# Kernel optimization log

Hardware: AMD Instinct MI355X
Metric: run time of the kernel (lower is better)

Reference implementation:

```python
import jax, jax.numpy as jnp
import numpy as np

T, N = 500, 20000
DT = 0.1
REST_CA = 0.0

PNAMES = ['decay_ca', 'rho_ca', 'p__tau', 'p__scale', 'p__mdp', 'q__tau', 'q__scale',
          'q__mdp', 'n__tau', 'n__scale', 'n__mdp', 'f__tau', 'f__scale', 'f__mdp',
          'e__tau', 'e__scale', 'e__mdp', 'h__alpha', 'h__scale', 'h__mdp',
          'C_m', 'g_Ca', 'g_Ks', 'g_Kf', 'g_L', 'E_Ca', 'E_K', 'E_L']
DEFAULT = {'decay_ca': 110.0, 'rho_ca': 0.23, 'p__tau': 100.0, 'p__scale': 7.43,
           'p__mdp': -8.05, 'q__tau': 150.0, 'q__scale': -9.97, 'q__mdp': -15.6,
           'n__tau': 25.0, 'n__scale': 15.9, 'n__mdp': 19.9, 'f__tau': 151.0,
           'f__scale': -5.03, 'f__mdp': 25.2, 'e__tau': 10.0, 'e__scale': 6.75,
           'e__mdp': -3.36, 'h__alpha': 0.282, 'h__scale': -1.0, 'h__mdp': 6.42,
           'C_m': 20.0, 'g_Ca': 3.0, 'g_Ks': 10.0, 'g_Kf': 0.07, 'g_L': 0.005,
           'E_Ca': 20.0, 'E_K': -60.0, 'E_L': -60.0}
# initial state: V, p, q, n, e, f, cac
INIT_STATE = [-50.0, 0.0, 0.95, 0.0, 0.0, 1.0, 1e-07]


def setup_inputs() -> dict:
    key = jax.random.key(0)
    # injected current per timestep and neuron (uA/cm^2)
    i_inj = jax.random.normal(key, (T, N), dtype=jnp.float32) * 2.0 + 5.0
    x0 = jnp.broadcast_to(jnp.asarray(INIT_STATE, dtype=jnp.float32)[:, None], (7, N))
    params = jnp.asarray([DEFAULT[k] for k in PNAMES], dtype=jnp.float32)
    return {'i_inj': i_inj, 'x0': x0, 'params': params}


def _simulate(i_inj, x0, params):
    P = {k: params[i] for i, k in enumerate(PNAMES)}
    dt = jnp.float32(DT)

    def inf(V, r):
        return jax.nn.sigmoid((V - P[r + '__mdp']) / P[r + '__scale'])

    def gate(x, V, r):
        tau = P[r + '__tau']
        return tau * dt / (tau + dt) * (x / dt + inf(V, r) / tau)

    def step(X, i):
        V, p, q, n, e, f, cac = X  # each [N]
        h = 1.0 + (jax.nn.sigmoid((cac - P['h__mdp']) / P['h__scale']) - 1.0) * P['h__alpha']
        i_ca = P['g_Ca'] * e ** 2 * f * h * (V - P['E_Ca'])
        i_ks = P['g_Ks'] * n * (V - P['E_K'])
        i_kf = P['g_Kf'] * p ** 4 * q * (V - P['E_K'])
        i_l = P['g_L'] * (V - P['E_L'])
        V = V + (i - i_ca - i_ks - i_kf - i_l) / P['C_m'] * dt
        # cac update uses I_Ca recomputed with the *updated* V (as in source)
        i_ca2 = P['g_Ca'] * e ** 2 * f * h * (V - P['E_Ca'])
        cac = cac + (-i_ca2 * P['rho_ca'] - (cac - REST_CA) / P['decay_ca']) * dt
        p = gate(p, V, 'p')
        q = gate(q, V, 'q')
        e = gate(e, V, 'e')
        f = gate(f, V, 'f')
        n = gate(n, V, 'n')
        Xn = jnp.stack([V, p, q, n, e, f, cac], 0)
        return Xn, Xn

    _, traj = jax.lax.scan(step, x0, i_inj)
    return traj  # [T, 7, N]


def reference(i_inj, x0, params):
    return _simulate(i_inj, x0, params)
```

## Files before the change

### kernel.cpp

```cpp
#include <hip/hip_runtime.h>
#include <hip/hip_bf16.h>


#define TSTEPS 500
#define NNEUR  20000
#define DTS    0.1f
#define LOG2E  1.442695040888963f

__device__ __forceinline__ float hw_exp2(float x) { return __builtin_amdgcn_exp2f(x); }
__device__ __forceinline__ float hw_rcp(float x)  { return __builtin_amdgcn_rcpf(x); }

__global__ __launch_bounds__(64, 1)
void hh_kernel(const float* __restrict__ i_inj,
               const float* __restrict__ x0,
               const float* __restrict__ prm,
               float* __restrict__ out)
{
    const int n = blockIdx.x * 64 + threadIdx.x;
    if (n >= NNEUR) return;

    const float decay_ca = prm[0],  rho_ca  = prm[1];
    const float p_tau = prm[2],  p_scale = prm[3],  p_mdp = prm[4];
    const float q_tau = prm[5],  q_scale = prm[6],  q_mdp = prm[7];
    const float n_tau = prm[8],  n_scale = prm[9],  n_mdp = prm[10];
    const float f_tau = prm[11], f_scale = prm[12], f_mdp = prm[13];
    const float e_tau = prm[14], e_scale = prm[15], e_mdp = prm[16];
    const float h_alpha = prm[17], h_scale = prm[18], h_mdp = prm[19];
    const float C_m = prm[20], g_Ca = prm[21], g_Ks = prm[22];
    const float g_Kf = prm[23], g_L = prm[24];
    const float E_Ca = prm[25], E_K = prm[26], E_L = prm[27];

    const float kV    = DTS / C_m;
    const float cLEL  = g_L * E_L;
    const float cKeep = 1.0f - DTS / decay_ca;
    const float cRho  = rho_ca * DTS;

    const float isH = 1.0f / h_scale;
    const float zaH = -LOG2E * isH, zbH = h_mdp * isH * LOG2E;
    const float aG  = h_alpha * g_Ca;
    const float bG  = (1.0f - h_alpha) * g_Ca;

#define GATECONST(r, tau, scale, mdp)                                          \
    const float cf_##r = (tau) * DTS / ((tau) + DTS);                          \
    const float A_##r  = cf_##r / DTS;                                         \
    const float B_##r  = cf_##r / (tau);                                       \
    const float za##r  = -LOG2E / (scale);                                     \
    const float zb##r  = (mdp) * LOG2E / (scale);
    GATECONST(p, p_tau, p_scale, p_mdp)
    GATECONST(q, q_tau, q_scale, q_mdp)
    GATECONST(n, n_tau, n_scale, n_mdp)
    GATECONST(f, f_tau, f_scale, f_mdp)
    GATECONST(e, e_tau, e_scale, e_mdp)
#undef GATECONST

    float V   = x0[0 * NNEUR + n];
    float p   = x0[1 * NNEUR + n];
    float q   = x0[2 * NNEUR + n];
    float nn  = x0[3 * NNEUR + n];
    float e   = x0[4 * NNEUR + n];
    float f   = x0[5 * NNEUR + n];
    float cac = x0[6 * NNEUR + n];

    float* const oV = out + 0 * NNEUR;
    float* const oP = out + 1 * NNEUR;
    float* const oQ = out + 2 * NNEUR;
    float* const oN = out + 3 * NNEUR;
    float* const oE = out + 4 * NNEUR;
    float* const oF = out + 5 * NNEUR;
    float* const oC = out + 6 * NNEUR;
    unsigned boff = (unsigned)n * 4u;
    const unsigned BSTEP = 7u * NNEUR * 4u;
    unsigned ioff = (unsigned)n * 4u;
    const unsigned ISTEP = (unsigned)NNEUR * 4u;

#define LD(off)  (*(const float*)((const char*)i_inj + (off)))
#define ST(ptr)  (*(float*)((char*)(ptr) + boff))

#define HH_STEP(cur)                                                           \
    {                                                                          \
                                      \
        const float hs  = hw_rcp(1.0f + hw_exp2(fmaf(cac, zaH, zbH)));         \
        const float hg  = fmaf(hs, aG, bG);                        \
        const float geh = (e * e) * (f * hg);                                  \
        const float p2  = p * p;                                               \
        const float g   = fmaf(g_Kf, (p2 * p2) * q, g_Ks * nn);                \
        const float gtot = geh + g + g_L;                                      \
        const float t3  = fmaf(g, E_K, fmaf(geh, E_Ca, (cur) + cLEL));         \
        const float num = fmaf(-gtot, V, t3);                                  \
        V = fmaf(num, kV, V);                                                  \
                                               \
        const float ica2 = geh * (V - E_Ca);                                   \
        cac = fmaf(cac, cKeep, -(ica2 * cRho));                                \
                                                       \
        const float sp = hw_rcp(1.0f + hw_exp2(fmaf(V, zap, zbp)));            \
        const float sq = hw_rcp(1.0f + hw_exp2(fmaf(V, zaq, zbq)));            \
        const float se = hw_rcp(1.0f + hw_exp2(fmaf(V, zae, zbe)));            \
        const float sf = hw_rcp(1.0f + hw_exp2(fmaf(V, zaf, zbf)));            \
        const float sn = hw_rcp(1.0f + hw_exp2(fmaf(V, zan, zbn)));            \
        p  = fmaf(A_p, p,  B_p * sp);                                          \
        q  = fmaf(A_q, q,  B_q * sq);                                          \
        e  = fmaf(A_e, e,  B_e * se);                                          \
        f  = fmaf(A_f, f,  B_f * sf);                                          \
        nn = fmaf(A_n, nn, B_n * sn);                                          \
        ST(oV) = V;  ST(oP) = p;  ST(oQ) = q;  ST(oN) = nn;                    \
        ST(oE) = e;  ST(oF) = f;  ST(oC) = cac;                                \
        boff += BSTEP;                                                         \
    }

    float buf[8];
#pragma unroll
    for (int j = 0; j < 8; ++j)
        buf[j] = LD(ioff + (unsigned)j * ISTEP);
    ioff += 8u * ISTEP;

    for (int t0 = 0; t0 < TSTEPS - 8; t0 += 8) {
        float nbuf[8];
#pragma unroll
        for (int j = 0; j < 8; ++j) {
            unsigned o = ioff + (unsigned)j * ISTEP;
            const unsigned omax = (unsigned)(TSTEPS - 1) * ISTEP + (unsigned)n * 4u;
            o = o < omax ? o : omax;
            nbuf[j] = LD(o);
        }
        ioff += 8u * ISTEP;
#pragma unroll
        for (int j = 0; j < 8; ++j)
            HH_STEP(buf[j]);
#pragma unroll
        for (int j = 0; j < 8; ++j)
            buf[j] = nbuf[j];
    }

#pragma unroll
    for (int j = 0; j < 4; ++j)
        HH_STEP(buf[j]);

#undef HH_STEP
#undef LD
#undef ST
}

extern "C" void kernel_launch(void* const* d_in, const int* in_sizes, int n_in,
                              void* d_out, int out_size, void* d_ws, size_t ws_size,
                              hipStream_t stream) {
    const float* i_inj  = (const float*)d_in[0];
    const float* x0     = (const float*)d_in[1];
    const float* params = (const float*)d_in[2];
    float* out = (float*)d_out;

    const int block = 64;
    const int grid  = (NNEUR + block - 1) / block;
    hipLaunchKernelGGL(hh_kernel, dim3(grid), dim3(block), 0, stream,
                       i_inj, x0, params, out);
}
```

Before: 360.8 us.

## Process four neurons per thread to interleave independent recurrence chains

Each thread now integrates four neurons spaced NT apart, interleaving their time steps so independent dependency chains overlap in the pipeline. The grid shrinks fourfold, and the input prefetch depth drops from 8 to 4 steps with a uniform loop. This trades occupancy and CU coverage (far fewer waves than CUs) for instruction-level parallelism inside each wave.

```diff
diff --git a/kernel.cpp b/kernel.cpp
--- a/kernel.cpp
+++ b/kernel.cpp
@@ -4,6 +4,8 @@
 
 #define TSTEPS 500
 #define NNEUR  20000
+#define KN     4
+#define NT     (NNEUR / KN)
 #define DTS    0.1f
 #define LOG2E  1.442695040888963f
 
@@ -17,7 +19,7 @@
                float* __restrict__ out)
 {
     const int n = blockIdx.x * 64 + threadIdx.x;
-    if (n >= NNEUR) return;
+    if (n >= NT) return;
 
     const float decay_ca = prm[0],  rho_ca  = prm[1];
     const float p_tau = prm[2],  p_scale = prm[3],  p_mdp = prm[4];
@@ -53,13 +55,18 @@
     GATECONST(e, e_tau, e_scale, e_mdp)
 #undef GATECONST
 
-    float V   = x0[0 * NNEUR + n];
-    float p   = x0[1 * NNEUR + n];
-    float q   = x0[2 * NNEUR + n];
-    float nn  = x0[3 * NNEUR + n];
-    float e   = x0[4 * NNEUR + n];
-    float f   = x0[5 * NNEUR + n];
-    float cac = x0[6 * NNEUR + n];
+    float V[KN], P[KN], Q[KN], NN[KN], E[KN], F[KN], C[KN];
+#pragma unroll
+    for (int k = 0; k < KN; ++k) {
+        const int nk = n + k * NT;
+        V[k]  = x0[0 * NNEUR + nk];
+        P[k]  = x0[1 * NNEUR + nk];
+        Q[k]  = x0[2 * NNEUR + nk];
+        NN[k] = x0[3 * NNEUR + nk];
+        E[k]  = x0[4 * NNEUR + nk];
+        F[k]  = x0[5 * NNEUR + nk];
+        C[k]  = x0[6 * NNEUR + nk];
+    }
 
     float* const oV = out + 0 * NNEUR;
     float* const oP = out + 1 * NNEUR;
@@ -68,72 +75,80 @@
     float* const oE = out + 4 * NNEUR;
     float* const oF = out + 5 * NNEUR;
     float* const oC = out + 6 * NNEUR;
-    unsigned boff = (unsigned)n * 4u;
+
+    const unsigned ISTEP = (unsigned)NNEUR * 4u;
     const unsigned BSTEP = 7u * NNEUR * 4u;
-    unsigned ioff = (unsigned)n * 4u;
-    const unsigned ISTEP = (unsigned)NNEUR * 4u;
+    unsigned bo[KN];
+    unsigned i0[KN];
+#pragma unroll
+    for (int k = 0; k < KN; ++k) {
+        bo[k] = (unsigned)(n + k * NT) * 4u;
+        i0[k] = (unsigned)(n + k * NT) * 4u;
+    }
 
-#define LD(off)  (*(const float*)((const char*)i_inj + (off)))
-#define ST(ptr)  (*(float*)((char*)(ptr) + boff))
+#define LD(off)      (*(const float*)((const char*)i_inj + (off)))
+#define ST(ptr, off) (*(float*)((char*)(ptr) + (off)))
 
-#define HH_STEP(cur)                                                           \
+#define HH_STEP(k, cur)                                                        \
     {                                                                          \
-                                      \
-        const float hs  = hw_rcp(1.0f + hw_exp2(fmaf(cac, zaH, zbH)));         \
-        const float hg  = fmaf(hs, aG, bG);                        \
-        const float geh = (e * e) * (f * hg);                                  \
-        const float p2  = p * p;                                               \
-        const float g   = fmaf(g_Kf, (p2 * p2) * q, g_Ks * nn);                \
+        const float hs  = hw_rcp(1.0f + hw_exp2(fmaf(C[k], zaH, zbH)));        \
+        const float hg  = fmaf(hs, aG, bG);                                    \
+        const float geh = (E[k] * E[k]) * (F[k] * hg);                         \
+        const float p2  = P[k] * P[k];                                         \
+        const float g   = fmaf(g_Kf, (p2 * p2) * Q[k], g_Ks * NN[k]);          \
         const float gtot = geh + g + g_L;                                      \
         const float t3  = fmaf(g, E_K, fmaf(geh, E_Ca, (cur) + cLEL));         \
-        const float num = fmaf(-gtot, V, t3);                                  \
-        V = fmaf(num, kV, V);                                                  \
-                                               \
-        const float ica2 = geh * (V - E_Ca);                                   \
-        cac = fmaf(cac, cKeep, -(ica2 * cRho));                                \
-                                                       \
-        const float sp = hw_rcp(1.0f + hw_exp2(fmaf(V, zap, zbp)));            \
-        const float sq = hw_rcp(1.0f + hw_exp2(fmaf(V, zaq, zbq)));            \
-        const float se = hw_rcp(1.0f + hw_exp2(fmaf(V, zae, zbe)));            \
-        const float sf = hw_rcp(1.0f + hw_exp2(fmaf(V, zaf, zbf)));            \
-        const float sn = hw_rcp(1.0f + hw_exp2(fmaf(V, zan, zbn)));            \
-        p  = fmaf(A_p, p,  B_p * sp);                                          \
-        q  = fmaf(A_q, q,  B_q * sq);                                          \
-        e  = fmaf(A_e, e,  B_e * se);                                          \
-        f  = fmaf(A_f, f,  B_f * sf);                                          \
-        nn = fmaf(A_n, nn, B_n * sn);                                          \
-        ST(oV) = V;  ST(oP) = p;  ST(oQ) = q;  ST(oN) = nn;                    \
-        ST(oE) = e;  ST(oF) = f;  ST(oC) = cac;                                \
-        boff += BSTEP;                                                         \
+        const float num = fmaf(-gtot, V[k], t3);                               \
+        V[k] = fmaf(num, kV, V[k]);                                            \
+        const float ica2 = geh * (V[k] - E_Ca);                                \
+        C[k] = fmaf(C[k], cKeep, -(ica2 * cRho));                              \
+        const float sp = hw_rcp(1.0f + hw_exp2(fmaf(V[k], zap, zbp)));         \
+        const float sq = hw_rcp(1.0f + hw_exp2(fmaf(V[k], zaq, zbq)));         \
+        const float se = hw_rcp(1.0f + hw_exp2(fmaf(V[k], zae, zbe)));         \
+        const float sf = hw_rcp(1.0f + hw_exp2(fmaf(V[k], zaf, zbf)));         \
+        const float sn = hw_rcp(1.0f + hw_exp2(fmaf(V[k], zan, zbn)));         \
+        P[k]  = fmaf(A_p, P[k],  B_p * sp);                                    \
+        Q[k]  = fmaf(A_q, Q[k],  B_q * sq);                                    \
+        E[k]  = fmaf(A_e, E[k],  B_e * se);                                    \
+        F[k]  = fmaf(A_f, F[k],  B_f * sf);                                    \
+        NN[k] = fmaf(A_n, NN[k], B_n * sn);                                    \
+        ST(oV, bo[k]) = V[k];  ST(oP, bo[k]) = P[k];                           \
+        ST(oQ, bo[k]) = Q[k];  ST(oN, bo[k]) = NN[k];                          \
+        ST(oE, bo[k]) = E[k];  ST(oF, bo[k]) = F[k];                           \
+        ST(oC, bo[k]) = C[k];                                                  \
+        bo[k] += BSTEP;                                                        \
     }
 
-    float buf[8];
-#pragma unroll
-    for (int j = 0; j < 8; ++j)
-        buf[j] = LD(ioff + (unsigned)j * ISTEP);
-    ioff += 8u * ISTEP;
-
-    for (int t0 = 0; t0 < TSTEPS - 8; t0 += 8) {
-        float nbuf[8];
-#pragma unroll
-        for (int j = 0; j < 8; ++j) {
-            unsigned o = ioff + (unsigned)j * ISTEP;
-            const unsigned omax = (unsigned)(TSTEPS - 1) * ISTEP + (unsigned)n * 4u;
-            o = o < omax ? o : omax;
-            nbuf[j] = LD(o);
-        }
-        ioff += 8u * ISTEP;
-#pragma unroll
-        for (int j = 0; j < 8; ++j)
-            HH_STEP(buf[j]);
-#pragma unroll
-        for (int j = 0; j < 8; ++j)
-            buf[j] = nbuf[j];
-    }
-
+    float buf[KN][4];
 #pragma unroll
     for (int j = 0; j < 4; ++j)
-        HH_STEP(buf[j]);
+#pragma unroll
+        for (int k = 0; k < KN; ++k)
+            buf[k][j] = LD(i0[k] + (unsigned)j * ISTEP);
+
+    for (int t0 = 0; t0 < TSTEPS; t0 += 4) {
+        float nbuf[KN][4];
+#pragma unroll
+        for (int j = 0; j < 4; ++j) {
+            int tt = t0 + 4 + j;
+            tt = tt < TSTEPS ? tt : TSTEPS - 1;
+            const unsigned ro = (unsigned)tt * ISTEP;
+#pragma unroll
+            for (int k = 0; k < KN; ++k)
+                nbuf[k][j] = LD(i0[k] + ro);
+        }
+#pragma unroll
+        for (int j = 0; j < 4; ++j) {
+#pragma unroll
+            for (int k = 0; k < KN; ++k)
+                HH_STEP(k, buf[k][j]);
+        }
+#pragma unroll
+        for (int j = 0; j < 4; ++j)
+#pragma unroll
+            for (int k = 0; k < KN; ++k)
+                buf[k][j] = nbuf[k][j];
+    }
 
 #undef HH_STEP
 #undef LD
@@ -149,7 +164,7 @@
     float* out = (float*)d_out;
 
     const int block = 64;
-    const int grid  = (NNEUR + block - 1) / block;
+    const int grid  = (NT + block - 1) / block;
     hipLaunchKernelGGL(hh_kernel, dim3(grid), dim3(block), 0, stream,
                        i_inj, x0, params, out);
 }
```

Measured after the change: 589.2 us. 63.3% more time.
